# Kernel optimization log

Hardware: AMD Instinct MI355X
Metric: run time of the kernel (lower is better)

The kernel has to match this reference:

```python
import jax, jax.numpy as jnp
import numpy as np

NUM_SCENES = 7
SHAPE = [512, 512, 256, 64]  # layer dims: 512->512->256->64
BATCH = 16384


def _xavier(key, shape):
    # nn.init.xavier_normal_ on (s, in, out): fan_in/fan_out from last two dims
    fan_in, fan_out = shape[-2], shape[-1]
    std = np.sqrt(2.0 / (fan_in + fan_out)).astype(np.float32)
    return jax.random.normal(key, shape, dtype=jnp.float32) * std


def setup_inputs() -> dict:
    key = jax.random.key(0)
    ks = jax.random.split(key, 16)
    inp = {
        "x": jax.random.normal(ks[0], (BATCH, SHAPE[0]), dtype=jnp.float32),
        "scene": jax.random.randint(ks[1], (BATCH,), 1, NUM_SCENES + 1, dtype=jnp.int64),
    }
    for i in range(3):
        din, dout = SHAPE[i], SHAPE[i + 1]
        inp[f"W{i}"] = _xavier(ks[2 + 4 * i], (NUM_SCENES, din, dout))
        inp[f"b{i}"] = jnp.zeros((NUM_SCENES, dout), dtype=jnp.float32)
        inp[f"gW{i}"] = _xavier(ks[3 + 4 * i], (1, din, dout))
        inp[f"gb{i}"] = jnp.zeros((1, dout), dtype=jnp.float32)
    return inp


def _star_linear(x, scene0, W, b, gW, gb, relu):
    # W: (S, in, out), gW: (1, in, out). Equivalent to gathering W[scene0]
    # and doing x[:,None,:] @ (w * gW), but computed as a dense GEMM over
    # all scenes followed by a per-sample select (avoids B*in*out gather).
    scaled = W * gW                                   # (S, in, out)
    out_all = jnp.einsum('bi,sio->bso', x, scaled)    # (B, S, out)
    out = jnp.take_along_axis(out_all, scene0[:, None, None], axis=1)[:, 0, :]
    out = out + b[scene0] + gb[0]
    if relu:
        out = jnp.maximum(out, 0.0)
    return out  # dropout is identity at eval


def reference(x, scene, W0, b0, gW0, gb0, W1, b1, gW1, gb1, W2, b2, gW2, gb2):
    scene0 = (scene - 1).astype(jnp.int32)
    h = _star_linear(x, scene0, W0, b0, gW0, gb0, relu=True)
    h = _star_linear(h, scene0, W1, b1, gW1, gb1, relu=True)
    h = _star_linear(h, scene0, W2, b2, gW2, gb2, relu=False)  # drop=True -> no relu
    return h
```

## Files before the change

kernel.cpp:

```cpp
#include <hip/hip_runtime.h>
#include <stdint.h>


#define BATCH   16384
#define NSCENE  7
#define TM      128
#define NBLK    (BATCH / 256)
#define MT_MAX  (BATCH / TM + NSCENE)
#define PADMAX  (BATCH + NSCENE * TM)

typedef __bf16 bf16x8 __attribute__((ext_vector_type(8)));
typedef float  f32x4  __attribute__((ext_vector_type(4)));

__device__ __forceinline__ ushort f2bf(float f) {
  union { float f; uint32_t u; } v; v.f = f;
  uint32_t r = (v.u + 0x7FFFu + ((v.u >> 16) & 1u)) >> 16;
  return (ushort)r;
}
__device__ __forceinline__ uint32_t pack2(float a, float b) {
  return (uint32_t)f2bf(a) | ((uint32_t)f2bf(b) << 16);
}

template<int K, int N>
__global__ void scale_transpose_k(const float* __restrict__ W,
                                  const float* __restrict__ gW,
                                  ushort* __restrict__ sT) {
  __shared__ float tl[32][33];
  int s = blockIdx.z;
  int n0 = blockIdx.x * 32, k0 = blockIdx.y * 32;
  int tx = threadIdx.x, ty = threadIdx.y;
  const float* Wp = W + (size_t)s * K * N;
#pragma unroll
  for (int i = 0; i < 4; i++) {
    int k = k0 + ty + i * 8;
    tl[ty + i * 8][tx] = Wp[(size_t)k * N + n0 + tx] * gW[(size_t)k * N + n0 + tx];
  }
  __syncthreads();
#pragma unroll
  for (int i = 0; i < 4; i++) {
    int n = n0 + ty + i * 8;
    sT[((size_t)s * N + n) * K + k0 + tx] = f2bf(tl[tx][ty + i * 8]);
  }
}

__global__ void bias_k(const float* __restrict__ b0, const float* __restrict__ gb0,
                       const float* __restrict__ b1, const float* __restrict__ gb1,
                       const float* __restrict__ b2, const float* __restrict__ gb2,
                       float* __restrict__ bias0, float* __restrict__ bias1,
                       float* __restrict__ bias2) {
  int t = blockIdx.x * 256 + threadIdx.x;
  if (t < 7 * 512) bias0[t] = b0[t] + gb0[t & 511];
  else if (t < 7 * 512 + 7 * 256) { int i = t - 7 * 512; bias1[i] = b1[i] + gb1[i & 255]; }
  else if (t < 7 * 512 + 7 * 256 + 7 * 64) { int i = t - 7 * 512 - 7 * 256; bias2[i] = b2[i] + gb2[i & 63]; }
}


__global__ void count_k(const int* __restrict__ scene, int* __restrict__ bcnt) {
  __shared__ int l[NSCENE];
  if (threadIdx.x < NSCENE) l[threadIdx.x] = 0;
  __syncthreads();
  int i = blockIdx.x * 256 + threadIdx.x;
  atomicAdd(&l[scene[i] - 1], 1);
  __syncthreads();
  if (threadIdx.x < NSCENE) bcnt[blockIdx.x * NSCENE + threadIdx.x] = l[threadIdx.x];
}

__global__ void plan_k(const int* __restrict__ bcnt, int* __restrict__ meta,
                       int* __restrict__ bbase) {
  __shared__ int tot[NSCENE];
  if (threadIdx.x < NSCENE) {
    int c = 0;
    for (int b = 0; b < NBLK; b++) c += bcnt[b * NSCENE + threadIdx.x];
    tot[threadIdx.x] = c;
  }
  __syncthreads();
  if (threadIdx.x == 0) {
    int po = 0, t = 0;
    for (int s = 0; s < NSCENE; s++) {
      meta[16 + s] = po;
      int tiles = (tot[s] + TM - 1) / TM;
      for (int j = 0; j < tiles; j++) { meta[32 + t] = s; meta[192 + t] = po + j * TM; t++; }
      po += tiles * TM;
    }
    meta[24] = t;
  }
  __syncthreads();
  if (threadIdx.x < NSCENE) {
    int s = threadIdx.x;
    int run = meta[16 + s];
    for (int b = 0; b < NBLK; b++) { bbase[b * NSCENE + s] = run; run += bcnt[b * NSCENE + s]; }
  }
}

__global__ void fill_k(int* __restrict__ idxp) {
  int i = blockIdx.x * 256 + threadIdx.x;
  if (i < PADMAX) idxp[i] = -1;
}

__global__ void scatter_k(const int* __restrict__ scene,
                          const int* __restrict__ bbase, int* __restrict__ idxp) {
  __shared__ int l[NSCENE];
  if (threadIdx.x < NSCENE) l[threadIdx.x] = 0;
  __syncthreads();
  int i = blockIdx.x * 256 + threadIdx.x;
  int s = scene[i] - 1;
  int pos = atomicAdd(&l[s], 1);
  idxp[bbase[blockIdx.x * NSCENE + s] + pos] = i;
}

template<int KDIM, int NDIM, int TN, bool GATHER_A, bool RELU, bool SCATTER_OUT>
__global__ __launch_bounds__(256) void gemm_k(
    const float* __restrict__ xin, const ushort* __restrict__ ain,
    const ushort* __restrict__ bw, const float* __restrict__ bias,
    const int* __restrict__ meta, const int* __restrict__ idxp,
    ushort* __restrict__ hout, float* __restrict__ out) {
  int t = blockIdx.x;
  if (t >= meta[24]) return;
  int sc = meta[32 + t];
  int mrow0 = meta[192 + t];
  int nb = blockIdx.y;

  constexpr int WN = TN / 2;
  constexpr int ACCN = WN / 16;

  __shared__ __align__(16) ushort Abuf[TM * 64];
  __shared__ __align__(16) ushort Bbuf[TN * 64];

  int tid = threadIdx.x;
  int lane = tid & 63, wid = tid >> 6;
  int wm = wid >> 1, wn = wid & 1;

  f32x4 acc[4][ACCN];
#pragma unroll
  for (int mt = 0; mt < 4; mt++)
#pragma unroll
    for (int nt = 0; nt < ACCN; nt++) acc[mt][nt] = (f32x4){0.f, 0.f, 0.f, 0.f};

  int idxc[4];
  if (GATHER_A) {
#pragma unroll
    for (int i = 0; i < 4; i++) idxc[i] = idxp[mrow0 + (tid >> 3) + i * 32];
  }

  const ushort* bwS = bw + ((size_t)sc * NDIM + (size_t)nb * TN) * KDIM;

  for (int kb = 0; kb < KDIM / 64; kb++) {
    if (GATHER_A) {
#pragma unroll
      for (int i = 0; i < 4; i++) {
        int c = tid + i * 256;
        int row = c >> 3, q = c & 7;
        int kcg = q ^ (row & 7);
        uint4 val;
        int g = idxc[i];
        if (g >= 0) {
          const float4* p = (const float4*)(xin + (size_t)g * 512 + kb * 64 + kcg * 8);
          float4 f0 = p[0], f1 = p[1];
          val.x = pack2(f0.x, f0.y); val.y = pack2(f0.z, f0.w);
          val.z = pack2(f1.x, f1.y); val.w = pack2(f1.z, f1.w);
        } else {
          val = make_uint4(0, 0, 0, 0);
        }
        *(uint4*)(&Abuf[c * 8]) = val;
      }
    } else {
#pragma unroll
      for (int i = 0; i < 4; i++) {
        int c = tid + i * 256;
        int row = c >> 3, q = c & 7;
        int kcg = q ^ (row & 7);
        *(uint4*)(&Abuf[c * 8]) =
            *(const uint4*)(ain + (size_t)(mrow0 + row) * KDIM + kb * 64 + kcg * 8);
      }
    }
#pragma unroll
    for (int i = 0; i < TN * 8 / 256; i++) {
      int c = tid + i * 256;
      int row = c >> 3, q = c & 7;
      int kcg = q ^ (row & 7);
      *(uint4*)(&Bbuf[c * 8]) =
          *(const uint4*)(bwS + (size_t)row * KDIM + kb * 64 + kcg * 8);
    }
    __syncthreads();
#pragma unroll
    for (int kk = 0; kk < 64; kk += 32) {
      bf16x8 af[4], bfr[ACCN];
      int kc = (kk >> 3) + (lane >> 4);
#pragma unroll
      for (int mt = 0; mt < 4; mt++) {
        int row = wm * 64 + mt * 16 + (lane & 15);
        af[mt] = *(const bf16x8*)(&Abuf[(row * 8 + (kc ^ (row & 7))) * 8]);
      }
#pragma unroll
      for (int nt = 0; nt < ACCN; nt++) {
        int row = wn * WN + nt * 16 + (lane & 15);
        bfr[nt] = *(const bf16x8*)(&Bbuf[(row * 8 + (kc ^ (row & 7))) * 8]);
      }
#pragma unroll
      for (int mt = 0; mt < 4; mt++)
#pragma unroll
        for (int nt = 0; nt < ACCN; nt++)
          acc[mt][nt] = __builtin_amdgcn_mfma_f32_16x16x32_bf16(af[mt], bfr[nt], acc[mt][nt], 0, 0, 0);
    }
    __syncthreads();
  }

  int gidx[4][4];
  if (SCATTER_OUT) {
#pragma unroll
    for (int mt = 0; mt < 4; mt++)
#pragma unroll
      for (int r = 0; r < 4; r++)
        gidx[mt][r] = idxp[mrow0 + wm * 64 + mt * 16 + (lane >> 4) * 4 + r];
  }
#pragma unroll
  for (int mt = 0; mt < 4; mt++) {
    int rl0 = wm * 64 + mt * 16 + (lane >> 4) * 4;
#pragma unroll
    for (int nt = 0; nt < ACCN; nt++) {
      int col = nb * TN + wn * WN + nt * 16 + (lane & 15);
      float bv = bias[sc * NDIM + col];
#pragma unroll
      for (int r = 0; r < 4; r++) {
        float v = acc[mt][nt][r] + bv;
        if (RELU) v = fmaxf(v, 0.f);
        if (SCATTER_OUT) {
          int g = gidx[mt][r];
          if (g >= 0) out[(size_t)g * NDIM + col] = v;
        } else {
          hout[(size_t)(mrow0 + rl0 + r) * NDIM + col] = f2bf(v);
        }
      }
    }
  }
}

extern "C" void kernel_launch(void* const* d_in, const int* in_sizes, int n_in,
                              void* d_out, int out_size, void* d_ws, size_t ws_size,
                              hipStream_t stream) {
  const float* x   = (const float*)d_in[0];
  const int* scene = (const int*)d_in[1];
  const float* W0  = (const float*)d_in[2];
  const float* b0  = (const float*)d_in[3];
  const float* gW0 = (const float*)d_in[4];
  const float* gb0 = (const float*)d_in[5];
  const float* W1  = (const float*)d_in[6];
  const float* b1  = (const float*)d_in[7];
  const float* gW1 = (const float*)d_in[8];
  const float* gb1 = (const float*)d_in[9];
  const float* W2  = (const float*)d_in[10];
  const float* b2  = (const float*)d_in[11];
  const float* gW2 = (const float*)d_in[12];
  const float* gb2 = (const float*)d_in[13];
  float* out = (float*)d_out;

  char* ws = (char*)d_ws;
  size_t off = 0;
  auto alloc = [&](size_t bytes) -> void* {
    void* p = ws + off;
    off = (off + bytes + 255) & ~(size_t)255;
    return p;
  };
  ushort* sT0   = (ushort*)alloc((size_t)7 * 512 * 512 * 2);
  ushort* sT1   = (ushort*)alloc((size_t)7 * 256 * 512 * 2);
  ushort* sT2   = (ushort*)alloc((size_t)7 * 64 * 256 * 2);
  float*  bias0 = (float*)alloc(7 * 512 * 4);
  float*  bias1 = (float*)alloc(7 * 256 * 4);
  float*  bias2 = (float*)alloc(7 * 64 * 4);
  int*    meta  = (int*)alloc(1024 * 4);
  int*    bcnt  = (int*)alloc(NBLK * NSCENE * 4);
  int*    bbase = (int*)alloc(NBLK * NSCENE * 4);
  int*    idxp  = (int*)alloc(PADMAX * 4);
  ushort* hc1   = (ushort*)alloc((size_t)PADMAX * 512 * 2);
  ushort* hc2   = (ushort*)alloc((size_t)PADMAX * 256 * 2);
  (void)ws_size; (void)n_in; (void)in_sizes; (void)out_size;

  scale_transpose_k<512, 512><<<dim3(16, 16, 7), dim3(32, 8), 0, stream>>>(W0, gW0, sT0);
  scale_transpose_k<512, 256><<<dim3(8, 16, 7), dim3(32, 8), 0, stream>>>(W1, gW1, sT1);
  scale_transpose_k<256, 64><<<dim3(2, 8, 7), dim3(32, 8), 0, stream>>>(W2, gW2, sT2);
  bias_k<<<dim3(23), 256, 0, stream>>>(b0, gb0, b1, gb1, b2, gb2, bias0, bias1, bias2);
  count_k<<<NBLK, 256, 0, stream>>>(scene, bcnt);
  plan_k<<<1, 256, 0, stream>>>(bcnt, meta, bbase);
  fill_k<<<(PADMAX + 255) / 256, 256, 0, stream>>>(idxp);
  scatter_k<<<NBLK, 256, 0, stream>>>(scene, bbase, idxp);

  gemm_k<512, 512, 128, true,  true,  false><<<dim3(MT_MAX, 4), 256, 0, stream>>>(
      x, nullptr, sT0, bias0, meta, idxp, hc1, nullptr);
  gemm_k<512, 256, 128, false, true,  false><<<dim3(MT_MAX, 2), 256, 0, stream>>>(
      nullptr, hc1, sT1, bias1, meta, idxp, hc2, nullptr);
  gemm_k<256, 64, 64,  false, false, true ><<<dim3(MT_MAX, 1), 256, 0, stream>>>(
      nullptr, hc2, sT2, bias2, meta, idxp, nullptr, out);
}
```

Before: 177.1 us.

## Merge prep kernels into one launch and use direct-to-LDS async loads in GEMM

Combines the three weight scale-transpose kernels, the bias kernel and the scene count kernel into a single prep launch dispatched by block index. The idx padding fill moves into plan_k, which now writes -1 only over the padded tail of each scene. The GEMM's non-gathered A and B tile loads use global_load_lds to write straight into shared memory without passing through registers, and the float-to-bf16 pack uses the HIP intrinsic. The aim is fewer launches and less register traffic in the GEMM main loop. The risk is that the async LDS destination addressing (a per-wave base) must match the swizzled layout, and no explicit wait is shown before the barrier.

```diff
diff --git a/kernel.cpp b/kernel.cpp
--- a/kernel.cpp
+++ b/kernel.cpp
@@ -1,4 +1,5 @@
 #include <hip/hip_runtime.h>
+#include <hip/hip_bf16.h>
 #include <stdint.h>
 
 
@@ -17,18 +18,24 @@
   uint32_t r = (v.u + 0x7FFFu + ((v.u >> 16) & 1u)) >> 16;
   return (ushort)r;
 }
-__device__ __forceinline__ uint32_t pack2(float a, float b) {
-  return (uint32_t)f2bf(a) | ((uint32_t)f2bf(b) << 16);
-}
-
-template<int K, int N>
-__global__ void scale_transpose_k(const float* __restrict__ W,
-                                  const float* __restrict__ gW,
-                                  ushort* __restrict__ sT) {
+__device__ __forceinline__ uint32_t pk2(float a, float b) {
+  union { __hip_bfloat162 h; uint32_t u; } cv;
+  cv.h = __float22bfloat162_rn(float2{a, b});
+  return cv.u;
+}
+__device__ __forceinline__ void async16(const void* g, void* lds) {
+  __builtin_amdgcn_global_load_lds(
+      (const __attribute__((address_space(1))) uint32_t*)g,
+      (__attribute__((address_space(3))) uint32_t*)lds, 16, 0, 0);
+}
+
+__device__ __forceinline__ void st_tile(const float* __restrict__ W,
+                                        const float* __restrict__ gW,
+                                        ushort* __restrict__ sT,
+                                        int K, int N, int s, int n0, int k0,
+                                        int tid) {
   __shared__ float tl[32][33];
-  int s = blockIdx.z;
-  int n0 = blockIdx.x * 32, k0 = blockIdx.y * 32;
-  int tx = threadIdx.x, ty = threadIdx.y;
+  int tx = tid & 31, ty = tid >> 5;
   const float* Wp = W + (size_t)s * K * N;
 #pragma unroll
   for (int i = 0; i < 4; i++) {
@@ -43,58 +50,78 @@
   }
 }
 
-__global__ void bias_k(const float* __restrict__ b0, const float* __restrict__ gb0,
-                       const float* __restrict__ b1, const float* __restrict__ gb1,
-                       const float* __restrict__ b2, const float* __restrict__ gb2,
-                       float* __restrict__ bias0, float* __restrict__ bias1,
-                       float* __restrict__ bias2) {
-  int t = blockIdx.x * 256 + threadIdx.x;
-  if (t < 7 * 512) bias0[t] = b0[t] + gb0[t & 511];
-  else if (t < 7 * 512 + 7 * 256) { int i = t - 7 * 512; bias1[i] = b1[i] + gb1[i & 255]; }
-  else if (t < 7 * 512 + 7 * 256 + 7 * 64) { int i = t - 7 * 512 - 7 * 256; bias2[i] = b2[i] + gb2[i & 63]; }
-}
-
-
-__global__ void count_k(const int* __restrict__ scene, int* __restrict__ bcnt) {
-  __shared__ int l[NSCENE];
-  if (threadIdx.x < NSCENE) l[threadIdx.x] = 0;
+#define NB_W0 (16 * 16 * 7)
+#define NB_W1 (8 * 16 * 7)
+#define NB_W2 (2 * 8 * 7)
+#define NB_BIAS 23
+#define NB_CNT NBLK
+
+__global__ __launch_bounds__(256) void prep_k(
+    const float* __restrict__ W0, const float* __restrict__ gW0,
+    const float* __restrict__ W1, const float* __restrict__ gW1,
+    const float* __restrict__ W2, const float* __restrict__ gW2,
+    const float* __restrict__ b0, const float* __restrict__ gb0,
+    const float* __restrict__ b1, const float* __restrict__ gb1,
+    const float* __restrict__ b2, const float* __restrict__ gb2,
+    const int* __restrict__ scene,
+    ushort* __restrict__ sT0, ushort* __restrict__ sT1, ushort* __restrict__ sT2,
+    float* __restrict__ bias0, float* __restrict__ bias1, float* __restrict__ bias2,
+    int* __restrict__ bcnt) {
+  int bid = blockIdx.x, tid = threadIdx.x;
+  if (bid < NB_W0) {
+    int l = bid;
+    st_tile(W0, gW0, sT0, 512, 512, l / 256, (l % 16) * 32, ((l / 16) % 16) * 32, tid);
+  } else if (bid < NB_W0 + NB_W1) {
+    int l = bid - NB_W0;
+    st_tile(W1, gW1, sT1, 512, 256, l / 128, (l % 8) * 32, ((l / 8) % 16) * 32, tid);
+  } else if (bid < NB_W0 + NB_W1 + NB_W2) {
+    int l = bid - NB_W0 - NB_W1;
+    st_tile(W2, gW2, sT2, 256, 64, l / 16, (l % 2) * 32, ((l / 2) % 8) * 32, tid);
+  } else if (bid < NB_W0 + NB_W1 + NB_W2 + NB_BIAS) {
+    int t = (bid - NB_W0 - NB_W1 - NB_W2) * 256 + tid;
+    if (t < 7 * 512) bias0[t] = b0[t] + gb0[t & 511];
+    else if (t < 7 * 512 + 7 * 256) { int i = t - 7 * 512; bias1[i] = b1[i] + gb1[i & 255]; }
+    else if (t < 7 * 512 + 7 * 256 + 7 * 64) { int i = t - 7 * 512 - 7 * 256; bias2[i] = b2[i] + gb2[i & 63]; }
+  } else {
+    __shared__ int l[NSCENE];
+    if (tid < NSCENE) l[tid] = 0;
+    __syncthreads();
+    int blk = bid - NB_W0 - NB_W1 - NB_W2 - NB_BIAS;
+    atomicAdd(&l[scene[blk * 256 + tid] - 1], 1);
+    __syncthreads();
+    if (tid < NSCENE) bcnt[blk * NSCENE + tid] = l[tid];
+  }
+}
+
+__global__ void plan_k(const int* __restrict__ bcnt, int* __restrict__ meta,
+                       int* __restrict__ bbase, int* __restrict__ idxp) {
+  __shared__ int tot[NSCENE], pstart[NSCENE], pend[NSCENE];
+  int tid = threadIdx.x;
+  if (tid < NSCENE) {
+    int c = 0;
+    for (int b = 0; b < NBLK; b++) c += bcnt[b * NSCENE + tid];
+    tot[tid] = c;
+  }
   __syncthreads();
-  int i = blockIdx.x * 256 + threadIdx.x;
-  atomicAdd(&l[scene[i] - 1], 1);
-  __syncthreads();
-  if (threadIdx.x < NSCENE) bcnt[blockIdx.x * NSCENE + threadIdx.x] = l[threadIdx.x];
-}
-
-__global__ void plan_k(const int* __restrict__ bcnt, int* __restrict__ meta,
-                       int* __restrict__ bbase) {
-  __shared__ int tot[NSCENE];
-  if (threadIdx.x < NSCENE) {
-    int c = 0;
-    for (int b = 0; b < NBLK; b++) c += bcnt[b * NSCENE + threadIdx.x];
-    tot[threadIdx.x] = c;
-  }
-  __syncthreads();
-  if (threadIdx.x == 0) {
+  if (tid == 0) {
     int po = 0, t = 0;
     for (int s = 0; s < NSCENE; s++) {
       meta[16 + s] = po;
       int tiles = (tot[s] + TM - 1) / TM;
+      pstart[s] = po + tot[s];
+      pend[s] = po + tiles * TM;
       for (int j = 0; j < tiles; j++) { meta[32 + t] = s; meta[192 + t] = po + j * TM; t++; }
       po += tiles * TM;
     }
     meta[24] = t;
   }
   __syncthreads();
-  if (threadIdx.x < NSCENE) {
-    int s = threadIdx.x;
-    int run = meta[16 + s];
-    for (int b = 0; b < NBLK; b++) { bbase[b * NSCENE + s] = run; run += bcnt[b * NSCENE + s]; }
-  }
-}
-
-__global__ void fill_k(int* __restrict__ idxp) {
-  int i = blockIdx.x * 256 + threadIdx.x;
-  if (i < PADMAX) idxp[i] = -1;
+  if (tid < NSCENE) {
+    int run = meta[16 + tid];
+    for (int b = 0; b < NBLK; b++) { bbase[b * NSCENE + tid] = run; run += bcnt[b * NSCENE + tid]; }
+  }
+  for (int s = 0; s < NSCENE; s++)
+    for (int i = pstart[s] + tid; i < pend[s]; i += 256) idxp[i] = -1;
 }
 
 __global__ void scatter_k(const int* __restrict__ scene,
@@ -150,14 +177,14 @@
       for (int i = 0; i < 4; i++) {
         int c = tid + i * 256;
         int row = c >> 3, q = c & 7;
-        int kcg = q ^ (row & 7);
+        int kg = q ^ (row & 7);
         uint4 val;
         int g = idxc[i];
         if (g >= 0) {
-          const float4* p = (const float4*)(xin + (size_t)g * 512 + kb * 64 + kcg * 8);
+          const float4* p = (const float4*)(xin + (size_t)g * 512 + kb * 64 + kg * 8);
           float4 f0 = p[0], f1 = p[1];
-          val.x = pack2(f0.x, f0.y); val.y = pack2(f0.z, f0.w);
-          val.z = pack2(f1.x, f1.y); val.w = pack2(f1.z, f1.w);
+          val.x = pk2(f0.x, f0.y); val.y = pk2(f0.z, f0.w);
+          val.z = pk2(f1.x, f1.y); val.w = pk2(f1.z, f1.w);
         } else {
           val = make_uint4(0, 0, 0, 0);
         }
@@ -168,18 +195,18 @@
       for (int i = 0; i < 4; i++) {
         int c = tid + i * 256;
         int row = c >> 3, q = c & 7;
-        int kcg = q ^ (row & 7);
-        *(uint4*)(&Abuf[c * 8]) =
-            *(const uint4*)(ain + (size_t)(mrow0 + row) * KDIM + kb * 64 + kcg * 8);
+        int kg = q ^ (row & 7);
+        async16(ain + (size_t)(mrow0 + row) * KDIM + kb * 64 + kg * 8,
+                &Abuf[(size_t)(i * 256 + wid * 64) * 8]);
       }
     }
 #pragma unroll
     for (int i = 0; i < TN * 8 / 256; i++) {
       int c = tid + i * 256;
       int row = c >> 3, q = c & 7;
-      int kcg = q ^ (row & 7);
-      *(uint4*)(&Bbuf[c * 8]) =
-          *(const uint4*)(bwS + (size_t)row * KDIM + kb * 64 + kcg * 8);
+      int kg = q ^ (row & 7);
+      async16(bwS + (size_t)row * KDIM + kb * 64 + kg * 8,
+              &Bbuf[(size_t)(i * 256 + wid * 64) * 8]);
     }
     __syncthreads();
 #pragma unroll
@@ -275,13 +302,10 @@
   ushort* hc2   = (ushort*)alloc((size_t)PADMAX * 256 * 2);
   (void)ws_size; (void)n_in; (void)in_sizes; (void)out_size;
 
-  scale_transpose_k<512, 512><<<dim3(16, 16, 7), dim3(32, 8), 0, stream>>>(W0, gW0, sT0);
-  scale_transpose_k<512, 256><<<dim3(8, 16, 7), dim3(32, 8), 0, stream>>>(W1, gW1, sT1);
-  scale_transpose_k<256, 64><<<dim3(2, 8, 7), dim3(32, 8), 0, stream>>>(W2, gW2, sT2);
-  bias_k<<<dim3(23), 256, 0, stream>>>(b0, gb0, b1, gb1, b2, gb2, bias0, bias1, bias2);
-  count_k<<<NBLK, 256, 0, stream>>>(scene, bcnt);
-  plan_k<<<1, 256, 0, stream>>>(bcnt, meta, bbase);
-  fill_k<<<(PADMAX + 255) / 256, 256, 0, stream>>>(idxp);
+  prep_k<<<NB_W0 + NB_W1 + NB_W2 + NB_BIAS + NB_CNT, 256, 0, stream>>>(
+      W0, gW0, W1, gW1, W2, gW2, b0, gb0, b1, gb1, b2, gb2, scene,
+      sT0, sT1, sT2, bias0, bias1, bias2, bcnt);
+  plan_k<<<1, 256, 0, stream>>>(bcnt, meta, bbase, idxp);
   scatter_k<<<NBLK, 256, 0, stream>>>(scene, bbase, idxp);
 
   gemm_k<512, 512, 128, true,  true,  false><<<dim3(MT_MAX, 4), 256, 0, stream>>>(
```

Result: faster. 166.7 us (-5.8%).
